# Kernel optimization log

Hardware: AMD Instinct MI355X
Metric: run time of the kernel (lower is better)

Reference implementation:

```python
import jax, jax.numpy as jnp
import numpy as np

CONFUSED_PAIRS = [(1, 2), (3, 4), (5, 6)]
NUM_CLASSES = 13
MARGIN = 0.5
IGNORE_INDEX = -100
BIG = 1e9  # finite sentinel instead of +/-inf (keeps grads clean)
EPS = 1e-12  # matches F.normalize eps

_conf_np = np.zeros((NUM_CLASSES, NUM_CLASSES), dtype=bool)
for _a, _b in CONFUSED_PAIRS:
    _conf_np[_a, _b] = True
    _conf_np[_b, _a] = True
CONF = jnp.asarray(_conf_np)  # [C, C] symmetric confused-class table


def setup_inputs() -> dict:
    key = jax.random.key(0)
    k1, k2 = jax.random.split(key)
    embeddings = jax.random.normal(k1, (16, 512, 256), dtype=jnp.float32)
    labels = jax.random.randint(k2, (16, 512), 0, 13, dtype=jnp.int64)
    return {"embeddings": embeddings, "labels": labels}


def reference(embeddings, labels):
    B, S, H = embeddings.shape
    e = embeddings.reshape(-1, H)                      # [N, H]
    lab = labels.reshape(-1)                           # [N]
    N = e.shape[0]

    valid = lab != IGNORE_INDEX                        # [N]
    # L2 normalize (F.normalize: divide by norm clamped to eps)
    norm = jnp.linalg.norm(e, axis=1, keepdims=True)
    e = e / jnp.maximum(norm, EPS)

    sim = e @ e.T                                      # [N, N] cosine sims

    lab_c = jnp.clip(lab, 0, NUM_CLASSES - 1)          # safe gather index
    # anchor label participates in some confused pair, and anchor is valid
    anchor_ok = valid & CONF[lab_c].any(axis=1)        # [N]

    same = lab[:, None] == lab[None, :]                # [N, N]
    eye = jnp.eye(N, dtype=bool)
    pos_mask = same & valid[None, :] & ~eye            # positives: same class, not self
    neg_mask = CONF[lab_c[:, None], lab_c[None, :]] & valid[None, :]  # confused-class negatives

    has_pos = pos_mask.any(axis=1)
    has_neg = neg_mask.any(axis=1)
    count_mask = anchor_ok & has_pos & has_neg         # [N] anchors contributing a triplet

    hardest_pos = jnp.min(jnp.where(pos_mask, sim, BIG), axis=1)   # [N]
    hardest_neg = jnp.max(jnp.where(neg_mask, sim, -BIG), axis=1)  # [N]

    triplet = jax.nn.relu(MARGIN + hardest_neg - hardest_pos)
    triplet = jnp.where(count_mask, triplet, 0.0)

    num_triplets = count_mask.sum()
    loss = triplet.sum() / jnp.maximum(num_triplets, 1).astype(triplet.dtype)
    return jnp.where(num_triplets > 0, loss, 0.0)
```

## Files before the change

### kernel.cpp

```cpp
#include <hip/hip_runtime.h>
#include <math.h>

#define Hdim    256
#define NMAX    8192
#define NPADMAX (NMAX + 6 * 32)
#define WLMAX   264
#define NSPLIT  2
#define SIMGRID 256
#define BIGV    1e9f
#define MARGIN  0.5f

typedef __attribute__((ext_vector_type(8))) short bf16x8;
typedef __attribute__((ext_vector_type(4))) float f32x4;

struct WS {
    unsigned short ebf[NMAX][Hdim];
    int idx[NPADMAX];
    int labG[NPADMAX];
    unsigned hpK[NPADMAX];
    unsigned hnK[NPADMAX];
    int S[8];
    int n[8];
    int wl_a[WLMAX];
    int wl_c[WLMAX];
    int T;
    unsigned done;
};

__device__ inline unsigned short f2bf(float f) {
    unsigned u = __float_as_uint(f);
    return (unsigned short)((u + 0x7fffu + ((u >> 16) & 1u)) >> 16);
}
__device__ inline unsigned fkey(float f) {
    unsigned u = __float_as_uint(f);
    return (u & 0x80000000u) ? ~u : (u | 0x80000000u);
}
__device__ inline float funkey(unsigned k) {
    unsigned u = (k & 0x80000000u) ? (k & 0x7fffffffu) : ~k;
    return __uint_as_float(u);
}

__global__ __launch_bounds__(256) void prep_kernel(const float* __restrict__ in,
                                                   const int* __restrict__ lab,
                                                   WS* ws, int N) {
    const int b = blockIdx.x, tid = threadIdx.x;
    if (b == 0) {
        __shared__ int h[8], S[8], cur[8];
        if (tid < 8) h[tid] = 0;
        __syncthreads();
        for (int i = tid; i < N; i += 256) {
            int l = lab[i];
            if (l >= 1 && l <= 6) atomicAdd(&h[l], 1);
        }
        __syncthreads();
        if (tid == 0) {
            int acc = 0; S[0] = 0;
            for (int c = 1; c <= 6; ++c) { S[c] = acc; acc += ((h[c] + 31) >> 5) << 5; }
            S[7] = acc;
            int T = 0;
            for (int c = 1; c <= 6; ++c) {
                int nt = (h[c] + 31) >> 5;
                for (int k = 0; k < nt; ++k) { ws->wl_a[T] = S[c] + 32 * k; ws->wl_c[T] = c; ++T; }
            }
            ws->T = T;
            ws->done = 0u;
            for (int c = 0; c < 8; ++c) { ws->n[c] = h[c]; ws->S[c] = S[c]; }
        }
        __syncthreads();
        const int SEnd = S[7];
        for (int g = tid; g < SEnd; g += 256) { ws->idx[g] = 0; ws->labG[g] = -1; }
        if (tid < 8) cur[tid] = S[tid];
        __syncthreads();
        for (int i = tid; i < N; i += 256) {
            int l = lab[i];
            if (l >= 1 && l <= 6) { int g = atomicAdd(&cur[l], 1); ws->idx[g] = i; ws->labG[g] = l; }
        }
    } else {
        const int wave = tid >> 6, lane = tid & 63;
        const int r0 = (b - 1) * 16 + wave * 4;
        #pragma unroll
        for (int k = 0; k < 4; ++k) {
            int row = r0 + k;
            if (row < N) {
                float4 v = ((const float4*)(in + (size_t)row * Hdim))[lane];
                float ss = v.x*v.x + v.y*v.y + v.z*v.z + v.w*v.w;
                #pragma unroll
                for (int off = 32; off >= 1; off >>= 1) ss += __shfl_xor(ss, off);
                float sc = 1.0f / fmaxf(sqrtf(ss), 1e-12f);
                ushort4 o;
                o.x = f2bf(v.x * sc); o.y = f2bf(v.y * sc);
                o.z = f2bf(v.z * sc); o.w = f2bf(v.w * sc);
                ((ushort4*)(&ws->ebf[row][0]))[lane] = o;
            }
        }
        if (tid < 17) {
            int g = (b - 1) * 17 + tid;
            if (g < NPADMAX) { ws->hpK[g] = 0xFFFFFFFFu; ws->hnK[g] = 0u; }
        }
    }
}

__global__ __launch_bounds__(256) void sim_kernel(WS* ws, float* __restrict__ out) {
    const int wave = threadIdx.x >> 6;
    const int lane = threadIdx.x & 63;
    const int col  = lane & 15;
    const int quad = lane >> 4;
    const int T    = ws->T;

    __shared__ float lds_hp[4][32], lds_hn[4][32];

    for (int w = blockIdx.x; w < T * NSPLIT; w += gridDim.x) {
        const int tileIdx = w >> 1, split = w & 1;
        const int aBase = ws->wl_a[tileIdx];
        const int c     = ws->wl_c[tileIdx];
        const int p     = ((c - 1) ^ 1) + 1;
        const int posS = ws->S[c], posRealE = posS + ws->n[c];
        const int negS = ws->S[p], negRealE = negS + ws->n[p];
        const int nPosT = (ws->S[c + 1] - posS) >> 4;
        const int nNegT = (ws->S[p + 1] - negS) >> 4;
        const int nTT   = nPosT + nNegT;

        const unsigned short* ebf = &ws->ebf[0][0];
        const int* __restrict__ idx = ws->idx;

        bf16x8 afrag[2][8];
        #pragma unroll
        for (int t2 = 0; t2 < 2; ++t2) {
            int row = idx[aBase + t2 * 16 + col];
            const unsigned short* rp = ebf + (size_t)row * Hdim + quad * 8;
            #pragma unroll
            for (int ks = 0; ks < 8; ++ks)
                afrag[t2][ks] = *(const bf16x8*)(rp + ks * 32);
        }

        float runMin[2][4], runMax[2][4];
        #pragma unroll
        for (int t2 = 0; t2 < 2; ++t2)
            #pragma unroll
            for (int r = 0; r < 4; ++r) { runMin[t2][r] = BIGV; runMax[t2][r] = -BIGV; }

        auto j0Of = [&](int t) -> int {
            return (t < nPosT) ? (posS + (t << 4)) : (negS + ((t - nPosT) << 4));
        };
        bf16x8 b0[8], b1[8];
        auto loadB = [&](bf16x8 (&bf)[8], int t) {
            int row = idx[j0Of(t) + col];
            const unsigned short* rp = ebf + (size_t)row * Hdim + quad * 8;
            #pragma unroll
            for (int ks = 0; ks < 8; ++ks)
                bf[ks] = *(const bf16x8*)(rp + ks * 32);
        };
        auto computeT = [&](bf16x8 (&bf)[8], int t) {
            int j0 = j0Of(t);
            bool isPos = t < nPosT;
            int realE  = isPos ? posRealE : negRealE;
            bool valid = (j0 + col) < realE;
            #pragma unroll
            for (int t2 = 0; t2 < 2; ++t2) {
                f32x4 acc = {0.f, 0.f, 0.f, 0.f};
                #pragma unroll
                for (int ks = 0; ks < 8; ++ks)
                    acc = __builtin_amdgcn_mfma_f32_16x16x32_bf16(afrag[t2][ks], bf[ks], acc, 0, 0, 0);
                if (isPos) {
                    #pragma unroll
                    for (int r = 0; r < 4; ++r)
                        runMin[t2][r] = fminf(runMin[t2][r], valid ? acc[r] : BIGV);
                } else {
                    #pragma unroll
                    for (int r = 0; r < 4; ++r)
                        runMax[t2][r] = fmaxf(runMax[t2][r], valid ? acc[r] : -BIGV);
                }
            }
        };

        const int first = split + NSPLIT * wave;
        int nIter = (nTT > first) ? ((nTT - first + 7) >> 3) : 0;
        int t = first, i = 0;
        if (nIter > 0) loadB(b0, t);
        while (i + 2 <= nIter) {
            loadB(b1, t + 8);
            computeT(b0, t);
            if (i + 2 < nIter) loadB(b0, t + 16);
            computeT(b1, t + 8);
            t += 16; i += 2;
        }
        if (i < nIter) computeT(b0, t);

        #pragma unroll
        for (int t2 = 0; t2 < 2; ++t2)
            #pragma unroll
            for (int r = 0; r < 4; ++r) {
                float mn = runMin[t2][r], mx = runMax[t2][r];
                #pragma unroll
                for (int off = 1; off < 16; off <<= 1) {
                    mn = fminf(mn, __shfl_xor(mn, off));
                    mx = fmaxf(mx, __shfl_xor(mx, off));
                }
                if (col == 0) {
                    int a = t2 * 16 + quad * 4 + r;
                    lds_hp[wave][a] = mn;
                    lds_hn[wave][a] = mx;
                }
            }
        __syncthreads();
        if (wave == 0 && lane < 32) {
            float hp = fminf(fminf(lds_hp[0][lane], lds_hp[1][lane]),
                             fminf(lds_hp[2][lane], lds_hp[3][lane]));
            float hn = fmaxf(fmaxf(lds_hn[0][lane], lds_hn[1][lane]),
                             fmaxf(lds_hn[2][lane], lds_hn[3][lane]));
            int a = aBase + lane;
            if (hp < 1e8f)  atomicMin(&ws->hpK[a], fkey(hp));
            if (hn > -1e8f) atomicMax(&ws->hnK[a], fkey(hn));
        }
        __syncthreads();
    }

    __shared__ unsigned oldv;
    if (threadIdx.x == 0) {
        __builtin_amdgcn_s_waitcnt(0);
        oldv = atomicAdd(&ws->done, 1u);
    }
    __syncthreads();
    if (oldv != (unsigned)(gridDim.x - 1)) return;
    __threadfence();

    __shared__ int ncls[8];
    if (threadIdx.x < 8) ncls[threadIdx.x] = ws->n[threadIdx.x];
    __syncthreads();
    float sum = 0.f; int cnt = 0;
    const int SEnd = ws->S[7];
    for (int g = threadIdx.x; g < SEnd; g += 256) {
        int l = ws->labG[g];
        if (l >= 1) {
            int p = ((l - 1) ^ 1) + 1;
            if (ncls[l] >= 2 && ncls[p] >= 1) {
                float hp = funkey(ws->hpK[g]);
                float hn = funkey(ws->hnK[g]);
                float tr = MARGIN + hn - hp;
                if (tr > 0.f) sum += tr;
                cnt += 1;
            }
        }
    }
    #pragma unroll
    for (int off = 32; off >= 1; off >>= 1) {
        sum += __shfl_xor(sum, off);
        cnt += __shfl_xor(cnt, off);
    }
    __shared__ float ssum[4]; __shared__ int scnt[4];
    if ((threadIdx.x & 63) == 0) { ssum[threadIdx.x >> 6] = sum; scnt[threadIdx.x >> 6] = cnt; }
    __syncthreads();
    if (threadIdx.x == 0) {
        float ts = ssum[0] + ssum[1] + ssum[2] + ssum[3];
        int   tc = scnt[0] + scnt[1] + scnt[2] + scnt[3];
        out[0] = (tc > 0) ? ts / (float)tc : 0.f;
    }
}

extern "C" void kernel_launch(void* const* d_in, const int* in_sizes, int n_in,
                              void* d_out, int out_size, void* d_ws, size_t ws_size,
                              hipStream_t stream) {
    const float* emb = (const float*)d_in[0];
    const int*   lab = (const int*)d_in[1];
    int N = in_sizes[1];
    WS* ws = (WS*)d_ws;

    prep_kernel<<<1 + (N + 15) / 16, 256, 0, stream>>>(emb, lab, ws, N);
    sim_kernel<<<SIMGRID, 256, 0, stream>>>(ws, (float*)d_out);
}
```

Before: 109.3 us.

## Store normalized rows in class-sorted order to drop indirect index gathers

```diff
diff --git a/kernel.cpp b/kernel.cpp
--- a/kernel.cpp
+++ b/kernel.cpp
@@ -14,8 +14,8 @@
 typedef __attribute__((ext_vector_type(4))) float f32x4;
 
 struct WS {
-    unsigned short ebf[NMAX][Hdim];
-    int idx[NPADMAX];
+    unsigned short ebf[NPADMAX][Hdim];
+    int gpos[NMAX];
     int labG[NPADMAX];
     unsigned hpK[NPADMAX];
     unsigned hnK[NPADMAX];
@@ -40,64 +40,87 @@
     return __uint_as_float(u);
 }
 
-__global__ __launch_bounds__(256) void prep_kernel(const float* __restrict__ in,
-                                                   const int* __restrict__ lab,
-                                                   WS* ws, int N) {
-    const int b = blockIdx.x, tid = threadIdx.x;
-    if (b == 0) {
-        __shared__ int h[8], S[8], cur[8];
-        if (tid < 8) h[tid] = 0;
-        __syncthreads();
-        for (int i = tid; i < N; i += 256) {
-            int l = lab[i];
-            if (l >= 1 && l <= 6) atomicAdd(&h[l], 1);
-        }
-        __syncthreads();
-        if (tid == 0) {
-            int acc = 0; S[0] = 0;
-            for (int c = 1; c <= 6; ++c) { S[c] = acc; acc += ((h[c] + 31) >> 5) << 5; }
-            S[7] = acc;
-            int T = 0;
-            for (int c = 1; c <= 6; ++c) {
-                int nt = (h[c] + 31) >> 5;
-                for (int k = 0; k < nt; ++k) { ws->wl_a[T] = S[c] + 32 * k; ws->wl_c[T] = c; ++T; }
-            }
-            ws->T = T;
-            ws->done = 0u;
-            for (int c = 0; c < 8; ++c) { ws->n[c] = h[c]; ws->S[c] = S[c]; }
-        }
-        __syncthreads();
-        const int SEnd = S[7];
-        for (int g = tid; g < SEnd; g += 256) { ws->idx[g] = 0; ws->labG[g] = -1; }
-        if (tid < 8) cur[tid] = S[tid];
-        __syncthreads();
-        for (int i = tid; i < N; i += 256) {
-            int l = lab[i];
-            if (l >= 1 && l <= 6) { int g = atomicAdd(&cur[l], 1); ws->idx[g] = i; ws->labG[g] = l; }
-        }
-    } else {
-        const int wave = tid >> 6, lane = tid & 63;
-        const int r0 = (b - 1) * 16 + wave * 4;
-        #pragma unroll
-        for (int k = 0; k < 4; ++k) {
-            int row = r0 + k;
-            if (row < N) {
-                float4 v = ((const float4*)(in + (size_t)row * Hdim))[lane];
-                float ss = v.x*v.x + v.y*v.y + v.z*v.z + v.w*v.w;
-                #pragma unroll
-                for (int off = 32; off >= 1; off >>= 1) ss += __shfl_xor(ss, off);
-                float sc = 1.0f / fmaxf(sqrtf(ss), 1e-12f);
-                ushort4 o;
-                o.x = f2bf(v.x * sc); o.y = f2bf(v.y * sc);
-                o.z = f2bf(v.z * sc); o.w = f2bf(v.w * sc);
-                ((ushort4*)(&ws->ebf[row][0]))[lane] = o;
-            }
-        }
-        if (tid < 17) {
-            int g = (b - 1) * 17 + tid;
-            if (g < NPADMAX) { ws->hpK[g] = 0xFFFFFFFFu; ws->hnK[g] = 0u; }
-        }
-    }
+__global__ __launch_bounds__(1024) void plan_kernel(const int* __restrict__ lab,
+                                                    WS* ws, int N) {
+    const int tid  = threadIdx.x;
+    const int wave = tid >> 6, lane = tid & 63;
+    __shared__ int wcnt[16][6];
+    __shared__ int S[8];
+    __shared__ int cur[6];
+
+    int cnt[6] = {0, 0, 0, 0, 0, 0};
+    for (int i = tid; i < N; i += 1024) {
+        int l = lab[i];
+        #pragma unroll
+        for (int c = 0; c < 6; ++c) cnt[c] += (l == c + 1);
+    }
+    #pragma unroll
+    for (int c = 0; c < 6; ++c) {
+        int v = cnt[c];
+        #pragma unroll
+        for (int off = 32; off >= 1; off >>= 1) v += __shfl_xor(v, off);
+        if (lane == 0) wcnt[wave][c] = v;
+    }
+    __syncthreads();
+    if (tid == 0) {
+        int h[6];
+        #pragma unroll
+        for (int c = 0; c < 6; ++c) { int s = 0; for (int w = 0; w < 16; ++w) s += wcnt[w][c]; h[c] = s; }
+        int acc = 0; S[0] = 0;
+        for (int c = 1; c <= 6; ++c) { S[c] = acc; acc += ((h[c - 1] + 31) >> 5) << 5; }
+        S[7] = acc;
+        int T = 0;
+        for (int c = 1; c <= 6; ++c) {
+            int nt = (h[c - 1] + 31) >> 5;
+            for (int k = 0; k < nt; ++k) { ws->wl_a[T] = S[c] + 32 * k; ws->wl_c[T] = c; ++T; }
+        }
+        ws->T = T;
+        ws->done = 0u;
+        ws->n[0] = 0; ws->n[7] = 0;
+        for (int c = 1; c <= 6; ++c) ws->n[c] = h[c - 1];
+        for (int c = 0; c < 8; ++c) ws->S[c] = S[c];
+    }
+    __syncthreads();
+    if (tid < 6) cur[tid] = S[tid + 1];
+    const int SEnd = S[7];
+    for (int g = tid; g < SEnd; g += 1024) {
+        ws->hpK[g] = 0xFFFFFFFFu; ws->hnK[g] = 0u; ws->labG[g] = -1;
+    }
+    __syncthreads();
+    for (int i = tid; i < N; i += 1024) {
+        int l = lab[i];
+        int g = -1;
+        #pragma unroll
+        for (int c = 1; c <= 6; ++c) {
+            unsigned long long mask = __ballot(l == c);
+            if (mask) {
+                int leader = __builtin_ctzll(mask);
+                int base = 0;
+                if (lane == leader) base = atomicAdd(&cur[c - 1], __popcll(mask));
+                base = __shfl(base, leader);
+                if (l == c) g = base + __popcll(mask & ((1ULL << lane) - 1ULL));
+            }
+        }
+        if (g >= 0) ws->labG[g] = l;
+        ws->gpos[i] = g;
+    }
+}
+
+__global__ __launch_bounds__(256) void norm_gather_kernel(const float* __restrict__ in,
+                                                          WS* ws) {
+    int row  = blockIdx.x * 4 + (threadIdx.x >> 6);
+    int lane = threadIdx.x & 63;
+    int g = ws->gpos[row];
+    if (g < 0) return;
+    float4 v = ((const float4*)(in + (size_t)row * Hdim))[lane];
+    float ss = v.x*v.x + v.y*v.y + v.z*v.z + v.w*v.w;
+    #pragma unroll
+    for (int off = 32; off >= 1; off >>= 1) ss += __shfl_xor(ss, off);
+    float sc = 1.0f / fmaxf(sqrtf(ss), 1e-12f);
+    ushort4 o;
+    o.x = f2bf(v.x * sc); o.y = f2bf(v.y * sc);
+    o.z = f2bf(v.z * sc); o.w = f2bf(v.w * sc);
+    ((ushort4*)(&ws->ebf[g][0]))[lane] = o;
 }
 
 __global__ __launch_bounds__(256) void sim_kernel(WS* ws, float* __restrict__ out) {
@@ -121,13 +144,11 @@
         const int nTT   = nPosT + nNegT;
 
         const unsigned short* ebf = &ws->ebf[0][0];
-        const int* __restrict__ idx = ws->idx;
 
         bf16x8 afrag[2][8];
         #pragma unroll
         for (int t2 = 0; t2 < 2; ++t2) {
-            int row = idx[aBase + t2 * 16 + col];
-            const unsigned short* rp = ebf + (size_t)row * Hdim + quad * 8;
+            const unsigned short* rp = ebf + (size_t)(aBase + t2 * 16 + col) * Hdim + quad * 8;
             #pragma unroll
             for (int ks = 0; ks < 8; ++ks)
                 afrag[t2][ks] = *(const bf16x8*)(rp + ks * 32);
@@ -144,8 +165,7 @@
         };
         bf16x8 b0[8], b1[8];
         auto loadB = [&](bf16x8 (&bf)[8], int t) {
-            int row = idx[j0Of(t) + col];
-            const unsigned short* rp = ebf + (size_t)row * Hdim + quad * 8;
+            const unsigned short* rp = ebf + (size_t)(j0Of(t) + col) * Hdim + quad * 8;
             #pragma unroll
             for (int ks = 0; ks < 8; ++ks)
                 bf[ks] = *(const bf16x8*)(rp + ks * 32);
@@ -265,6 +285,7 @@
     int N = in_sizes[1];
     WS* ws = (WS*)d_ws;
 
-    prep_kernel<<<1 + (N + 15) / 16, 256, 0, stream>>>(emb, lab, ws, N);
+    plan_kernel<<<1, 1024, 0, stream>>>(lab, ws, N);
+    norm_gather_kernel<<<(N + 3) / 4, 256, 0, stream>>>(emb, ws);
     sim_kernel<<<SIMGRID, 256, 0, stream>>>(ws, (float*)d_out);
 }
```

Measured after the change: 106.3 us. -2.8%, faster.
